# Optimization experiments

Hardware: AMD Instinct MI355X
Metric: run time of the kernel (lower is better)

Reference implementation:

```python
import jax, jax.numpy as jnp
import numpy as np

N = 100000
E = 6400000
GAMMA = 1.0
SUPPORT = 0.05


def cohesion_kernel(q, h):
    # piecewise Akinci cohesion kernel (Cd normalization is unused in the original)
    qm1_3_q3 = (q - 1.0) ** 3 * q ** 3
    k1 = 128.0 * qm1_3_q3 + 1.0   # q <= 0.5
    k2 = 64.0 * qm1_3_q3           # q > 0.5
    return -jnp.where(q <= 0.5, k1, k2)


def kernel_gradient(q, dist, h):
    # 2D Wendland C2 kernel gradient: W = 7/(pi h^2) (1-q)^4 (1+4q)
    C = 7.0 / (np.pi * h ** 2)
    dWdq = C * (-20.0 * q * jnp.clip(1.0 - q, 0.0, None) ** 3) / h
    return dWdq[:, None] * dist  # [E,2]


def setup_inputs() -> dict:
    key = jax.random.key(0)
    k1, k2, k3, k4, k5, k6, k7 = jax.random.split(key, 7)
    neighbors = jnp.stack([
        jax.random.randint(k1, (E,), 0, N),
        jax.random.randint(k2, (E,), 0, N),
    ], axis=0)  # [2,E] int
    fluidAreas = jax.random.uniform(k3, (N,), dtype=jnp.float32)
    fluidDensities = jax.random.uniform(k4, (N,), dtype=jnp.float32) + 0.5  # avoid div-by-0
    fluidRestDensity = jax.random.uniform(k5, (N,), dtype=jnp.float32) + 0.5
    fluidRadialDistances = jax.random.uniform(k6, (E,), dtype=jnp.float32)  # q in [0,1]
    fluidDistances = jax.random.normal(k7, (E, 2), dtype=jnp.float32)
    # normalize to unit direction vectors as in the SPH pipeline
    fluidDistances = fluidDistances / (jnp.linalg.norm(fluidDistances, axis=1, keepdims=True) + 1e-7)
    return {
        'neighbors': neighbors,
        'fluidAreas': fluidAreas,
        'fluidDensities': fluidDensities,
        'fluidRestDensity': fluidRestDensity,
        'fluidRadialDistances': fluidRadialDistances,
        'fluidDistances': fluidDistances,
    }


def reference(neighbors, fluidAreas, fluidDensities, fluidRestDensity,
              fluidRadialDistances, fluidDistances):
    i = neighbors[0]
    j = neighbors[1]

    # computeNormalFunction
    fac_n = fluidAreas[j] / fluidDensities[j]                  # [E]
    grad = kernel_gradient(fluidRadialDistances, fluidDistances, SUPPORT)  # [E,2]
    normals = SUPPORT * jax.ops.segment_sum(fac_n[:, None] * grad, i, num_segments=N)  # [N,2]

    # computeCurvatureForce
    curvature = -GAMMA * jax.ops.segment_sum(normals[i] - normals[j], i, num_segments=N)

    # computeCohesionForce
    fac_c = fluidAreas[j] * fluidRestDensity[j]                # [E]
    kern = cohesion_kernel(fluidRadialDistances, SUPPORT)      # [E]
    cohesion = -GAMMA * jax.ops.segment_sum((fac_c * kern)[:, None] * fluidDistances, i, num_segments=N)

    # both forces are accumulated into fluidAcceleration
    return curvature + cohesion
```

## Files before the change

### kernel.cpp

```cpp
#include <hip/hip_runtime.h>

constexpr int N_PART = 100000;
constexpr int N_EDGE = 6400000;
constexpr float SUPPORT = 0.05f;
constexpr float PI_F = 3.14159265358979323846f;

constexpr int CH_LOG2 = 12;
constexpr int CH      = 1 << CH_LOG2;
constexpr int NCH     = (N_EDGE + CH - 1) / CH;
constexpr int BIN_LOG2 = 13;
constexpr int BINSZ   = 1 << BIN_LOG2;
constexpr int NBIN    = (N_PART + BINSZ - 1) / BINSZ;
constexpr int G_MAX   = 39;
constexpr int ST_NW   = 8;

__global__ __launch_bounds__(512) void prep_fac(
    const float* __restrict__ areas,
    const float* __restrict__ dens,
    const float* __restrict__ rest,
    float2* __restrict__ fac)
{
    int p = blockIdx.x * blockDim.x + threadIdx.x;
    if (p < N_PART)
        fac[p] = make_float2(areas[p] / dens[p], areas[p] * rest[p]);
}

__global__ __launch_bounds__(512) void l1_sort(
    const int* __restrict__ nb,
    const float2* __restrict__ fac,
    const float* __restrict__ q,
    const float2* __restrict__ dist,
    unsigned* __restrict__ gpack,
    float2* __restrict__ gpay1,
    float2* __restrict__ gpay2,
    unsigned* __restrict__ btab)
{
    __shared__ unsigned rec_pack[CH];
    __shared__ float    rec_q[CH];
    __shared__ float    rec_dx[CH];
    __shared__ float    rec_dy[CH];
    __shared__ unsigned hist[ST_NW * NBIN];
    __shared__ unsigned curw[ST_NW * NBIN];
    __shared__ unsigned base[NBIN + 1];
    __shared__ unsigned bcnt[NBIN];

    const int t   = blockIdx.x;
    const int c0  = t * CH;
    const int len = min(CH, N_EDGE - c0);
    const int tid = threadIdx.x;
    const int wid = tid >> 6;

    for (int k = tid; k < ST_NW * NBIN; k += 512) hist[k] = 0u;

    unsigned iv[8], jv[8];
    float    qv[8], dxv[8], dyv[8];
    #pragma unroll
    for (int k = 0; k < 8; ++k) {
        int idx = tid + k * 512;
        if (idx < len) {
            iv[k] = (unsigned)nb[c0 + idx];
            jv[k] = (unsigned)nb[N_EDGE + c0 + idx];
            qv[k] = q[c0 + idx];
            float2 d = dist[c0 + idx];
            dxv[k] = d.x;
            dyv[k] = d.y;
        }
    }
    __syncthreads();

    #pragma unroll
    for (int k = 0; k < 8; ++k) {
        int idx = tid + k * 512;
        if (idx < len)
            atomicAdd(&hist[wid * NBIN + (iv[k] >> BIN_LOG2)], 1u);
    }
    __syncthreads();

    if (tid < NBIN) {
        unsigned run = 0;
        for (int w = 0; w < ST_NW; ++w) {
            curw[w * NBIN + tid] = run;
            run += hist[w * NBIN + tid];
        }
        bcnt[tid] = run;
    }
    __syncthreads();
    if (tid == 0) {
        unsigned run = 0;
        for (int b = 0; b < NBIN; ++b) { base[b] = run; run += bcnt[b]; }
        base[NBIN] = run;
    }
    __syncthreads();
    if (tid < ST_NW * NBIN) curw[tid] += base[tid % NBIN];
    if (tid < NBIN)  btab[t * 16 + tid]  = base[tid];
    if (tid == NBIN) btab[t * 16 + NBIN] = (unsigned)len;
    __syncthreads();

    #pragma unroll
    for (int k = 0; k < 8; ++k) {
        int idx = tid + k * 512;
        if (idx < len) {
            unsigned i   = iv[k];
            unsigned bin = i >> BIN_LOG2;
            unsigned r = atomicAdd(&curw[wid * NBIN + bin], 1u) & (CH - 1);
            rec_pack[r] = ((i & (BINSZ - 1)) << 17) | jv[k];
            rec_q[r]    = qv[k];
            rec_dx[r]   = dxv[k];
            rec_dy[r]   = dyv[k];
        }
    }
    __syncthreads();

    const float Cw = 7.0f / (PI_F * SUPPORT * SUPPORT);
    for (int p = tid; p < len; p += 512) {
        unsigned pack = rec_pack[p];
        float qq = rec_q[p];
        float dx = rec_dx[p], dy = rec_dy[p];
        unsigned j = pack & 0x1FFFFu;
        float2 f = fac[j];

        float omq  = fmaxf(1.0f - qq, 0.0f);
        float dWdq = Cw * (-20.0f * qq * omq * omq * omq) * (1.0f / SUPPORT);
        float s    = SUPPORT * f.x * dWdq;

        float qm1  = qq - 1.0f;
        float tt   = qm1 * qm1 * qm1 * qq * qq * qq;
        float kern = (qq <= 0.5f) ? fmaf(128.0f, tt, 1.0f) : 64.0f * tt;
        float fc   = f.y * kern;

        int o = c0 + p;
        gpack[o] = pack;
        gpay1[o] = make_float2(s * dx, s * dy);
        gpay2[o] = make_float2(fc * dx, fc * dy);
    }
}

__global__ __launch_bounds__(512) void passB(
    const unsigned* __restrict__ btab,
    const unsigned* __restrict__ gpack,
    const float2* __restrict__ gpay1,
    float2* __restrict__ partials,
    int G)
{
    __shared__ float accx[BINSZ];
    __shared__ float accy[BINSZ];
    const int b = blockIdx.x % NBIN;
    const int g = blockIdx.x / NBIN;
    const int wave = threadIdx.x >> 6;
    const int lane = threadIdx.x & 63;

    for (int k = threadIdx.x; k < BINSZ; k += 512) { accx[k] = 0.0f; accy[k] = 0.0f; }
    __syncthreads();

    const int t0 = (int)((long long)g * NCH / G);
    const int t1 = (int)((long long)(g + 1) * NCH / G);
    for (int t = t0 + wave; t < t1; t += 8) {
        const int c0  = t * CH;
        const unsigned ln = min(btab[t * 16 + NBIN], (unsigned)CH);
        unsigned sb = min(btab[t * 16 + b], ln);
        unsigned se = min(btab[t * 16 + b + 1], ln);
        for (unsigned k = sb + lane; k < se; k += 64) {
            int o = c0 + (int)k;
            unsigned pk = gpack[o];
            float2 p = gpay1[o];
            unsigned loc = (pk >> 17) & (BINSZ - 1);
            atomicAdd(&accx[loc], p.x);
            atomicAdd(&accy[loc], p.y);
        }
    }
    __syncthreads();

    float2* __restrict__ dst = partials + (size_t)g * (NBIN * BINSZ) + (size_t)b * BINSZ;
    for (int k = threadIdx.x; k < BINSZ; k += 512)
        dst[k] = make_float2(accx[k], accy[k]);
}

__global__ __launch_bounds__(512) void passD(
    const unsigned* __restrict__ btab,
    const unsigned* __restrict__ gpack,
    const float2* __restrict__ gpay2,
    const float2* __restrict__ normals,
    float2* __restrict__ partials,
    int G)
{
    __shared__ float accx[BINSZ];
    __shared__ float accy[BINSZ];
    const int b = blockIdx.x % NBIN;
    const int g = blockIdx.x / NBIN;
    const int wave = threadIdx.x >> 6;
    const int lane = threadIdx.x & 63;

    for (int k = threadIdx.x; k < BINSZ; k += 512) { accx[k] = 0.0f; accy[k] = 0.0f; }
    __syncthreads();

    const int gbase = b * BINSZ;
    const int t0 = (int)((long long)g * NCH / G);
    const int t1 = (int)((long long)(g + 1) * NCH / G);
    for (int t = t0 + wave; t < t1; t += 8) {
        const int c0  = t * CH;
        const unsigned ln = min(btab[t * 16 + NBIN], (unsigned)CH);
        unsigned sb = min(btab[t * 16 + b], ln);
        unsigned se = min(btab[t * 16 + b + 1], ln);
        for (unsigned k = sb + lane; k < se; k += 64) {
            int o = c0 + (int)k;
            unsigned pk = gpack[o];
            float2 coh = gpay2[o];
            unsigned loc = (pk >> 17) & (BINSZ - 1);
            unsigned j   = min(pk & 0x1FFFFu, (unsigned)(N_PART - 1));
            unsigned ii  = min((unsigned)(gbase + loc), (unsigned)(N_PART - 1));
            float2 nj = normals[j];
            float2 ni = normals[ii];
            atomicAdd(&accx[loc], nj.x - ni.x + coh.x);
            atomicAdd(&accy[loc], nj.y - ni.y + coh.y);
        }
    }
    __syncthreads();

    float2* __restrict__ dst = partials + (size_t)g * (NBIN * BINSZ) + (size_t)b * BINSZ;
    for (int k = threadIdx.x; k < BINSZ; k += 512)
        dst[k] = make_float2(accx[k], accy[k]);
}

__global__ __launch_bounds__(256) void reduceG(
    const float2* __restrict__ partials, float2* __restrict__ dst, int G)
{
    int p = blockIdx.x * blockDim.x + threadIdx.x;
    if (p >= N_PART) return;
    float ax = 0.0f, ay = 0.0f;
    for (int g = 0; g < G; ++g) {
        float2 v = partials[(size_t)g * (NBIN * BINSZ) + p];
        ax += v.x; ay += v.y;
    }
    dst[p] = make_float2(ax, ay);
}

constexpr int FB_BSZ_LOG2 = 13;
constexpr int FB_BSZ   = 1 << FB_BSZ_LOG2;
constexpr int FB_NBINS = (N_PART + FB_BSZ - 1) / FB_BSZ;
constexpr int FB_NP_PAD = FB_NBINS * FB_BSZ;
constexpr int FB_C_TARGET = 39;

__global__ __launch_bounds__(1024) void fb_pass1_binned(
    const int* __restrict__ nb, const float* __restrict__ areas,
    const float* __restrict__ dens, const float* __restrict__ q,
    const float2* __restrict__ dist, float* __restrict__ partials, int C)
{
    __shared__ float lds[2 * FB_BSZ];
    const int b = blockIdx.x % FB_NBINS;
    const int c = blockIdx.x / FB_NBINS;
    for (int k = threadIdx.x; k < 2 * FB_BSZ; k += blockDim.x) lds[k] = 0.0f;
    __syncthreads();
    const int start = (int)((long long)c       * (N_EDGE / 4) / C) * 4;
    const int end   = (int)((long long)(c + 1) * (N_EDGE / 4) / C) * 4;
    const int4* __restrict__ nb4 = (const int4*)nb;
    const float Cw = 7.0f / (PI_F * SUPPORT * SUPPORT);
    for (int e = start + (int)threadIdx.x * 4; e < end; e += (int)blockDim.x * 4) {
        int4 iq = nb4[e >> 2];
        #pragma unroll
        for (int k = 0; k < 4; ++k) {
            int iv = (k == 0) ? iq.x : (k == 1) ? iq.y : (k == 2) ? iq.z : iq.w;
            if ((iv >> FB_BSZ_LOG2) == b) {
                int ee = e + k;
                int j  = nb[N_EDGE + ee];
                float qq  = q[ee];
                float fac = areas[j] / dens[j];
                float omq  = fmaxf(1.0f - qq, 0.0f);
                float dWdq = Cw * (-20.0f * qq * omq * omq * omq) * (1.0f / SUPPORT);
                float s = SUPPORT * fac * dWdq;
                float2 d = dist[ee];
                int loc = (iv & (FB_BSZ - 1)) << 1;
                atomicAdd(&lds[loc],     s * d.x);
                atomicAdd(&lds[loc + 1], s * d.y);
            }
        }
    }
    __syncthreads();
    float2* __restrict__ dst = (float2*)partials + (size_t)c * FB_NP_PAD + (size_t)b * FB_BSZ;
    const float2* __restrict__ src = (const float2*)lds;
    for (int k = threadIdx.x; k < FB_BSZ; k += blockDim.x) dst[k] = src[k];
}

__global__ __launch_bounds__(1024) void fb_pass2_binned(
    const int* __restrict__ nb, const float* __restrict__ areas,
    const float* __restrict__ rest, const float* __restrict__ q,
    const float2* __restrict__ dist, const float2* __restrict__ normals,
    float* __restrict__ partials, int C)
{
    __shared__ float lds[2 * FB_BSZ];
    const int b = blockIdx.x % FB_NBINS;
    const int c = blockIdx.x / FB_NBINS;
    for (int k = threadIdx.x; k < 2 * FB_BSZ; k += blockDim.x) lds[k] = 0.0f;
    __syncthreads();
    const int start = (int)((long long)c       * (N_EDGE / 4) / C) * 4;
    const int end   = (int)((long long)(c + 1) * (N_EDGE / 4) / C) * 4;
    const int4* __restrict__ nb4 = (const int4*)nb;
    for (int e = start + (int)threadIdx.x * 4; e < end; e += (int)blockDim.x * 4) {
        int4 iq = nb4[e >> 2];
        #pragma unroll
        for (int k = 0; k < 4; ++k) {
            int iv = (k == 0) ? iq.x : (k == 1) ? iq.y : (k == 2) ? iq.z : iq.w;
            if ((iv >> FB_BSZ_LOG2) == b) {
                int ee = e + k;
                int j  = nb[N_EDGE + ee];
                float2 ni = normals[iv];
                float2 nj = normals[j];
                float qq  = q[ee];
                float fc  = areas[j] * rest[j];
                float qm1 = qq - 1.0f;
                float t   = qm1 * qm1 * qm1 * qq * qq * qq;
                float kern = (qq <= 0.5f) ? fmaf(128.0f, t, 1.0f) : 64.0f * t;
                float2 d = dist[ee];
                int loc = (iv & (FB_BSZ - 1)) << 1;
                atomicAdd(&lds[loc],     -(ni.x - nj.x) + fc * kern * d.x);
                atomicAdd(&lds[loc + 1], -(ni.y - nj.y) + fc * kern * d.y);
            }
        }
    }
    __syncthreads();
    float2* __restrict__ dst = (float2*)partials + (size_t)c * FB_NP_PAD + (size_t)b * FB_BSZ;
    const float2* __restrict__ src = (const float2*)lds;
    for (int k = threadIdx.x; k < FB_BSZ; k += blockDim.x) dst[k] = src[k];
}

__global__ __launch_bounds__(256) void fb_reduce_partials(
    const float* __restrict__ partials, float* __restrict__ dst, int C)
{
    int p = blockIdx.x * blockDim.x + threadIdx.x;
    if (p >= N_PART) return;
    const float2* __restrict__ p2 = (const float2*)partials;
    float ax = 0.0f, ay = 0.0f;
    for (int c = 0; c < C; ++c) {
        float2 v = p2[(size_t)c * FB_NP_PAD + p];
        ax += v.x; ay += v.y;
    }
    ((float2*)dst)[p] = make_float2(ax, ay);
}

__global__ __launch_bounds__(256) void fb_zero2(float* __restrict__ a,
                                                float* __restrict__ b, int n) {
    int idx = blockIdx.x * blockDim.x + threadIdx.x;
    if (idx < n) { a[idx] = 0.0f; b[idx] = 0.0f; }
}

__global__ __launch_bounds__(256) void fb_pass1_atomic(
    const int* __restrict__ nb, const float* __restrict__ areas,
    const float* __restrict__ dens, const float* __restrict__ q,
    const float2* __restrict__ dist, float* __restrict__ normals)
{
    int e = blockIdx.x * blockDim.x + threadIdx.x;
    if (e >= N_EDGE) return;
    int i = nb[e];
    int j = nb[N_EDGE + e];
    float qq  = q[e];
    float fac = areas[j] / dens[j];
    const float Cw = 7.0f / (PI_F * SUPPORT * SUPPORT);
    float omq  = fmaxf(1.0f - qq, 0.0f);
    float dWdq = Cw * (-20.0f * qq * omq * omq * omq) * (1.0f / SUPPORT);
    float s = SUPPORT * fac * dWdq;
    float2 d = dist[e];
    atomicAdd(&normals[2 * i],     s * d.x);
    atomicAdd(&normals[2 * i + 1], s * d.y);
}

__global__ __launch_bounds__(256) void fb_pass2_atomic(
    const int* __restrict__ nb, const float* __restrict__ areas,
    const float* __restrict__ rest, const float* __restrict__ q,
    const float2* __restrict__ dist, const float2* __restrict__ normals,
    float* __restrict__ out)
{
    int e = blockIdx.x * blockDim.x + threadIdx.x;
    if (e >= N_EDGE) return;
    int i = nb[e];
    int j = nb[N_EDGE + e];
    float2 ni = normals[i];
    float2 nj = normals[j];
    float qq  = q[e];
    float fc  = areas[j] * rest[j];
    float qm1 = qq - 1.0f;
    float t   = qm1 * qm1 * qm1 * qq * qq * qq;
    float kern = (qq <= 0.5f) ? fmaf(128.0f, t, 1.0f) : 64.0f * t;
    float2 d = dist[e];
    atomicAdd(&out[2 * i],     -(ni.x - nj.x) + fc * kern * d.x);
    atomicAdd(&out[2 * i + 1], -(ni.y - nj.y) + fc * kern * d.y);
}

extern "C" void kernel_launch(void* const* d_in, const int* in_sizes, int n_in,
                              void* d_out, int out_size, void* d_ws, size_t ws_size,
                              hipStream_t stream) {
    const int*   nb    = (const int*)d_in[0];
    const float* areas = (const float*)d_in[1];
    const float* dens  = (const float*)d_in[2];
    const float* rest  = (const float*)d_in[3];
    const float* q     = (const float*)d_in[4];
    const float* dist  = (const float*)d_in[5];
    float* out = (float*)d_out;

    size_t off = 0;
    auto take = [&](size_t bytes) { size_t o = off; off += (bytes + 255) & ~(size_t)255; return o; };
    size_t o_pack    = take((size_t)N_EDGE * sizeof(unsigned));
    size_t o_pay1    = take((size_t)N_EDGE * sizeof(float2));
    size_t o_pay2    = take((size_t)N_EDGE * sizeof(float2));
    size_t o_btab    = take((size_t)NCH * 16 * sizeof(unsigned));
    size_t o_normals = take((size_t)N_PART * sizeof(float2));
    size_t o_fac     = take((size_t)N_PART * sizeof(float2));
    size_t base_need = off;
    const size_t per_g = (size_t)(NBIN * BINSZ) * sizeof(float2);

    int G = 0;
    if (ws_size > base_need) {
        G = (int)((ws_size - base_need) / per_g);
        if (G > G_MAX) G = G_MAX;
    }

    char* ws = (char*)d_ws;

    if (G >= 6) {
        unsigned* gpack   = (unsigned*)(ws + o_pack);
        float2*   gpay1   = (float2*)(ws + o_pay1);
        float2*   gpay2   = (float2*)(ws + o_pay2);
        unsigned* btab    = (unsigned*)(ws + o_btab);
        float2*   normals = (float2*)(ws + o_normals);
        float2*   fac     = (float2*)(ws + o_fac);
        float2*   partials= (float2*)(ws + base_need);

        prep_fac<<<(N_PART + 511) / 512, 512, 0, stream>>>(areas, dens, rest, fac);
        l1_sort<<<NCH, 512, 0, stream>>>(
            nb, fac, q, (const float2*)dist,
            gpack, gpay1, gpay2, btab);
        passB<<<NBIN * G, 512, 0, stream>>>(btab, gpack, gpay1, partials, G);
        reduceG<<<(N_PART + 255) / 256, 256, 0, stream>>>(partials, normals, G);
        passD<<<NBIN * G, 512, 0, stream>>>(btab, gpack, gpay2, normals, partials, G);
        reduceG<<<(N_PART + 255) / 256, 256, 0, stream>>>(partials, (float2*)out, G);
        return;
    }

    const size_t normals_pad = 1 << 20;
    float* normals  = (float*)d_ws;
    float* partials = (float*)((char*)d_ws + normals_pad);
    const size_t per_chunk = (size_t)FB_NP_PAD * 2 * sizeof(float);
    int C = 0;
    if (ws_size > normals_pad) {
        C = (int)((ws_size - normals_pad) / per_chunk);
        if (C > FB_C_TARGET) C = FB_C_TARGET;
    }

    if (C >= 4) {
        const int grid = FB_NBINS * C;
        fb_pass1_binned<<<grid, 1024, 0, stream>>>(
            nb, areas, dens, q, (const float2*)dist, partials, C);
        fb_reduce_partials<<<(N_PART + 255) / 256, 256, 0, stream>>>(partials, normals, C);
        fb_pass2_binned<<<grid, 1024, 0, stream>>>(
            nb, areas, rest, q, (const float2*)dist, (const float2*)normals, partials, C);
        fb_reduce_partials<<<(N_PART + 255) / 256, 256, 0, stream>>>(partials, out, C);
    } else {
        const int nv = 2 * N_PART;
        fb_zero2<<<(nv + 255) / 256, 256, 0, stream>>>(normals, out, nv);
        const int blocks = (N_EDGE + 255) / 256;
        fb_pass1_atomic<<<blocks, 256, 0, stream>>>(
            nb, areas, dens, q, (const float2*)dist, normals);
        fb_pass2_atomic<<<blocks, 256, 0, stream>>>(
            nb, areas, rest, q, (const float2*)dist, (const float2*)normals, out);
    }
}
```

Baseline: 373.9 us.

## Replace partial buffers and reduce kernels with global atomic flush; halve bin size

The binned accumulation passes now flush their LDS accumulators straight into the global normals and output arrays with atomicAdd, instead of writing per-group partial buffers and running separate reduceG kernels. The bin size drops from 8192 to 4096, doubling the bin count and halving LDS per block. Each block also stages its per-chunk bin offsets in LDS. This removes two kernel launches and the partial-buffer traffic, at the cost of a zeroing kernel, global atomic contention across the fixed 40 groups, and non-deterministic summation order.

```diff
diff --git a/kernel.cpp b/kernel.cpp
--- a/kernel.cpp
+++ b/kernel.cpp
@@ -8,11 +8,13 @@
 constexpr int CH_LOG2 = 12;
 constexpr int CH      = 1 << CH_LOG2;
 constexpr int NCH     = (N_EDGE + CH - 1) / CH;
-constexpr int BIN_LOG2 = 13;
+constexpr int BIN_LOG2 = 12;
 constexpr int BINSZ   = 1 << BIN_LOG2;
 constexpr int NBIN    = (N_PART + BINSZ - 1) / BINSZ;
-constexpr int G_MAX   = 39;
+constexpr int BT_STRIDE = 32;
+constexpr int G_ACC   = 40;
 constexpr int ST_NW   = 8;
+constexpr int MAXC    = 48;
 
 __global__ __launch_bounds__(512) void prep_fac(
     const float* __restrict__ areas,
@@ -23,6 +25,12 @@
     int p = blockIdx.x * blockDim.x + threadIdx.x;
     if (p < N_PART)
         fac[p] = make_float2(areas[p] / dens[p], areas[p] * rest[p]);
+}
+
+__global__ __launch_bounds__(256) void zero2(float* __restrict__ a,
+                                             float* __restrict__ b, int n) {
+    int idx = blockIdx.x * blockDim.x + threadIdx.x;
+    if (idx < n) { a[idx] = 0.0f; b[idx] = 0.0f; }
 }
 
 __global__ __launch_bounds__(512) void l1_sort(
@@ -92,8 +100,8 @@
     }
     __syncthreads();
     if (tid < ST_NW * NBIN) curw[tid] += base[tid % NBIN];
-    if (tid < NBIN)  btab[t * 16 + tid]  = base[tid];
-    if (tid == NBIN) btab[t * 16 + NBIN] = (unsigned)len;
+    if (tid < NBIN)  btab[t * BT_STRIDE + tid]  = base[tid];
+    if (tid == NBIN) btab[t * BT_STRIDE + NBIN] = (unsigned)len;
     __syncthreads();
 
     #pragma unroll
@@ -139,26 +147,33 @@
     const unsigned* __restrict__ btab,
     const unsigned* __restrict__ gpack,
     const float2* __restrict__ gpay1,
-    float2* __restrict__ partials,
-    int G)
+    float* __restrict__ gnorm)
 {
     __shared__ float accx[BINSZ];
     __shared__ float accy[BINSZ];
+    __shared__ unsigned s_sb[MAXC], s_se[MAXC], s_ln[MAXC];
     const int b = blockIdx.x % NBIN;
     const int g = blockIdx.x / NBIN;
     const int wave = threadIdx.x >> 6;
     const int lane = threadIdx.x & 63;
 
+    const int t0 = (int)((long long)g * NCH / G_ACC);
+    const int t1 = (int)((long long)(g + 1) * NCH / G_ACC);
+    const int nt = t1 - t0;
+
     for (int k = threadIdx.x; k < BINSZ; k += 512) { accx[k] = 0.0f; accy[k] = 0.0f; }
-    __syncthreads();
-
-    const int t0 = (int)((long long)g * NCH / G);
-    const int t1 = (int)((long long)(g + 1) * NCH / G);
-    for (int t = t0 + wave; t < t1; t += 8) {
-        const int c0  = t * CH;
-        const unsigned ln = min(btab[t * 16 + NBIN], (unsigned)CH);
-        unsigned sb = min(btab[t * 16 + b], ln);
-        unsigned se = min(btab[t * 16 + b + 1], ln);
+    for (int c = threadIdx.x; c < nt; c += 512) {
+        s_sb[c] = btab[(t0 + c) * BT_STRIDE + b];
+        s_se[c] = btab[(t0 + c) * BT_STRIDE + b + 1];
+        s_ln[c] = btab[(t0 + c) * BT_STRIDE + NBIN];
+    }
+    __syncthreads();
+
+    for (int c = wave; c < nt; c += 8) {
+        const int c0  = (t0 + c) * CH;
+        const unsigned ln = min(s_ln[c], (unsigned)CH);
+        unsigned sb = min(s_sb[c], ln);
+        unsigned se = min(s_se[c], ln);
         for (unsigned k = sb + lane; k < se; k += 64) {
             int o = c0 + (int)k;
             unsigned pk = gpack[o];
@@ -170,9 +185,14 @@
     }
     __syncthreads();
 
-    float2* __restrict__ dst = partials + (size_t)g * (NBIN * BINSZ) + (size_t)b * BINSZ;
-    for (int k = threadIdx.x; k < BINSZ; k += 512)
-        dst[k] = make_float2(accx[k], accy[k]);
+    const int gbase = b * BINSZ;
+    for (int k = threadIdx.x; k < BINSZ; k += 512) {
+        int p = gbase + k;
+        if (p < N_PART) {
+            atomicAdd(&gnorm[2 * p],     accx[k]);
+            atomicAdd(&gnorm[2 * p + 1], accy[k]);
+        }
+    }
 }
 
 __global__ __launch_bounds__(512) void passD(
@@ -180,27 +200,34 @@
     const unsigned* __restrict__ gpack,
     const float2* __restrict__ gpay2,
     const float2* __restrict__ normals,
-    float2* __restrict__ partials,
-    int G)
+    float* __restrict__ gout)
 {
     __shared__ float accx[BINSZ];
     __shared__ float accy[BINSZ];
+    __shared__ unsigned s_sb[MAXC], s_se[MAXC], s_ln[MAXC];
     const int b = blockIdx.x % NBIN;
     const int g = blockIdx.x / NBIN;
     const int wave = threadIdx.x >> 6;
     const int lane = threadIdx.x & 63;
 
+    const int t0 = (int)((long long)g * NCH / G_ACC);
+    const int t1 = (int)((long long)(g + 1) * NCH / G_ACC);
+    const int nt = t1 - t0;
+
     for (int k = threadIdx.x; k < BINSZ; k += 512) { accx[k] = 0.0f; accy[k] = 0.0f; }
+    for (int c = threadIdx.x; c < nt; c += 512) {
+        s_sb[c] = btab[(t0 + c) * BT_STRIDE + b];
+        s_se[c] = btab[(t0 + c) * BT_STRIDE + b + 1];
+        s_ln[c] = btab[(t0 + c) * BT_STRIDE + NBIN];
+    }
     __syncthreads();
 
     const int gbase = b * BINSZ;
-    const int t0 = (int)((long long)g * NCH / G);
-    const int t1 = (int)((long long)(g + 1) * NCH / G);
-    for (int t = t0 + wave; t < t1; t += 8) {
-        const int c0  = t * CH;
-        const unsigned ln = min(btab[t * 16 + NBIN], (unsigned)CH);
-        unsigned sb = min(btab[t * 16 + b], ln);
-        unsigned se = min(btab[t * 16 + b + 1], ln);
+    for (int c = wave; c < nt; c += 8) {
+        const int c0  = (t0 + c) * CH;
+        const unsigned ln = min(s_ln[c], (unsigned)CH);
+        unsigned sb = min(s_sb[c], ln);
+        unsigned se = min(s_se[c], ln);
         for (unsigned k = sb + lane; k < se; k += 64) {
             int o = c0 + (int)k;
             unsigned pk = gpack[o];
@@ -216,22 +243,13 @@
     }
     __syncthreads();
 
-    float2* __restrict__ dst = partials + (size_t)g * (NBIN * BINSZ) + (size_t)b * BINSZ;
-    for (int k = threadIdx.x; k < BINSZ; k += 512)
-        dst[k] = make_float2(accx[k], accy[k]);
-}
-
-__global__ __launch_bounds__(256) void reduceG(
-    const float2* __restrict__ partials, float2* __restrict__ dst, int G)
-{
-    int p = blockIdx.x * blockDim.x + threadIdx.x;
-    if (p >= N_PART) return;
-    float ax = 0.0f, ay = 0.0f;
-    for (int g = 0; g < G; ++g) {
-        float2 v = partials[(size_t)g * (NBIN * BINSZ) + p];
-        ax += v.x; ay += v.y;
-    }
-    dst[p] = make_float2(ax, ay);
+    for (int k = threadIdx.x; k < BINSZ; k += 512) {
+        int p = gbase + k;
+        if (p < N_PART) {
+            atomicAdd(&gout[2 * p],     accx[k]);
+            atomicAdd(&gout[2 * p + 1], accy[k]);
+        }
+    }
 }
 
 constexpr int FB_BSZ_LOG2 = 13;
@@ -336,12 +354,6 @@
     ((float2*)dst)[p] = make_float2(ax, ay);
 }
 
-__global__ __launch_bounds__(256) void fb_zero2(float* __restrict__ a,
-                                                float* __restrict__ b, int n) {
-    int idx = blockIdx.x * blockDim.x + threadIdx.x;
-    if (idx < n) { a[idx] = 0.0f; b[idx] = 0.0f; }
-}
-
 __global__ __launch_bounds__(256) void fb_pass1_atomic(
     const int* __restrict__ nb, const float* __restrict__ areas,
     const float* __restrict__ dens, const float* __restrict__ q,
@@ -400,37 +412,29 @@
     size_t o_pack    = take((size_t)N_EDGE * sizeof(unsigned));
     size_t o_pay1    = take((size_t)N_EDGE * sizeof(float2));
     size_t o_pay2    = take((size_t)N_EDGE * sizeof(float2));
-    size_t o_btab    = take((size_t)NCH * 16 * sizeof(unsigned));
+    size_t o_btab    = take((size_t)NCH * BT_STRIDE * sizeof(unsigned));
     size_t o_normals = take((size_t)N_PART * sizeof(float2));
     size_t o_fac     = take((size_t)N_PART * sizeof(float2));
     size_t base_need = off;
-    const size_t per_g = (size_t)(NBIN * BINSZ) * sizeof(float2);
-
-    int G = 0;
-    if (ws_size > base_need) {
-        G = (int)((ws_size - base_need) / per_g);
-        if (G > G_MAX) G = G_MAX;
-    }
 
     char* ws = (char*)d_ws;
 
-    if (G >= 6) {
+    if (ws_size >= base_need) {
         unsigned* gpack   = (unsigned*)(ws + o_pack);
         float2*   gpay1   = (float2*)(ws + o_pay1);
         float2*   gpay2   = (float2*)(ws + o_pay2);
         unsigned* btab    = (unsigned*)(ws + o_btab);
         float2*   normals = (float2*)(ws + o_normals);
         float2*   fac     = (float2*)(ws + o_fac);
-        float2*   partials= (float2*)(ws + base_need);
-
+
+        zero2<<<(2 * N_PART + 255) / 256, 256, 0, stream>>>(
+            (float*)normals, out, 2 * N_PART);
         prep_fac<<<(N_PART + 511) / 512, 512, 0, stream>>>(areas, dens, rest, fac);
         l1_sort<<<NCH, 512, 0, stream>>>(
             nb, fac, q, (const float2*)dist,
             gpack, gpay1, gpay2, btab);
-        passB<<<NBIN * G, 512, 0, stream>>>(btab, gpack, gpay1, partials, G);
-        reduceG<<<(N_PART + 255) / 256, 256, 0, stream>>>(partials, normals, G);
-        passD<<<NBIN * G, 512, 0, stream>>>(btab, gpack, gpay2, normals, partials, G);
-        reduceG<<<(N_PART + 255) / 256, 256, 0, stream>>>(partials, (float2*)out, G);
+        passB<<<NBIN * G_ACC, 512, 0, stream>>>(btab, gpack, gpay1, (float*)normals);
+        passD<<<NBIN * G_ACC, 512, 0, stream>>>(btab, gpack, gpay2, normals, out);
         return;
     }
 
@@ -454,7 +458,7 @@
         fb_reduce_partials<<<(N_PART + 255) / 256, 256, 0, stream>>>(partials, out, C);
     } else {
         const int nv = 2 * N_PART;
-        fb_zero2<<<(nv + 255) / 256, 256, 0, stream>>>(normals, out, nv);
+        zero2<<<(nv + 255) / 256, 256, 0, stream>>>(normals, out, nv);
         const int blocks = (N_EDGE + 255) / 256;
         fb_pass1_atomic<<<blocks, 256, 0, stream>>>(
             nb, areas, dens, q, (const float2*)dist, normals);
```

Measured after the change: 389.0 us. +4.0%, slower.

## Halve bin size, use wave-ballot ranking, stage chunk offsets, unroll scatter loops

Applied to the files above, without the earlier changes.

Bins shrink from 8192 to 4096 particles, so there are 25 bins and each accumulation block holds smaller LDS arrays, which may allow more blocks per CU. The btab stride grows to 32 to fit the extra bins. In the sort kernel, the shared-memory atomic histogram and the atomic position counter are replaced by deterministic ballot/mbcnt ranking per wave, with per-k prefix tables held in LDS. The passB and passD kernels now preload each chunk's bin start and end offsets into LDS and unroll the edge loop by two to issue more loads at once. The costs are a longer per-element bin loop in the sort kernel, twice as many blocks in passB and passD, and less headroom in the G/MAXC sizing.

```diff
diff --git a/kernel.cpp b/kernel.cpp
--- a/kernel.cpp
+++ b/kernel.cpp
@@ -8,11 +8,13 @@
 constexpr int CH_LOG2 = 12;
 constexpr int CH      = 1 << CH_LOG2;
 constexpr int NCH     = (N_EDGE + CH - 1) / CH;
-constexpr int BIN_LOG2 = 13;
+constexpr int BIN_LOG2 = 12;
 constexpr int BINSZ   = 1 << BIN_LOG2;
 constexpr int NBIN    = (N_PART + BINSZ - 1) / BINSZ;
-constexpr int G_MAX   = 39;
+constexpr int BT_STRIDE = 32;
+constexpr int G_MAX   = 40;
 constexpr int ST_NW   = 8;
+constexpr int MAXC    = 272;
 
 __global__ __launch_bounds__(512) void prep_fac(
     const float* __restrict__ areas,
@@ -40,7 +42,8 @@
     __shared__ float    rec_dx[CH];
     __shared__ float    rec_dy[CH];
     __shared__ unsigned hist[ST_NW * NBIN];
-    __shared__ unsigned curw[ST_NW * NBIN];
+    __shared__ unsigned wbase[ST_NW * NBIN];
+    __shared__ unsigned kpre[ST_NW * 8 * NBIN];
     __shared__ unsigned base[NBIN + 1];
     __shared__ unsigned bcnt[NBIN];
 
@@ -49,8 +52,7 @@
     const int len = min(CH, N_EDGE - c0);
     const int tid = threadIdx.x;
     const int wid = tid >> 6;
-
-    for (int k = tid; k < ST_NW * NBIN; k += 512) hist[k] = 0u;
+    const int lane = tid & 63;
 
     unsigned iv[8], jv[8];
     float    qv[8], dxv[8], dyv[8];
@@ -66,20 +68,31 @@
             dyv[k] = d.y;
         }
     }
-    __syncthreads();
-
+
+    unsigned rnk[8];
+    unsigned cntb = 0;
     #pragma unroll
     for (int k = 0; k < 8; ++k) {
         int idx = tid + k * 512;
-        if (idx < len)
-            atomicAdd(&hist[wid * NBIN + (iv[k] >> BIN_LOG2)], 1u);
-    }
+        unsigned bin = (idx < len) ? (iv[k] >> BIN_LOG2) : 0xFFu;
+        if (lane < NBIN) kpre[(wid * 8 + k) * NBIN + lane] = cntb;
+        unsigned r = 0;
+        for (unsigned b = 0; b < (unsigned)NBIN; ++b) {
+            unsigned long long m = __ballot(bin == b);
+            unsigned lt = __builtin_amdgcn_mbcnt_hi((unsigned)(m >> 32),
+                          __builtin_amdgcn_mbcnt_lo((unsigned)m, 0u));
+            if (bin == b) r = lt;
+            if ((unsigned)lane == b) cntb += (unsigned)__popcll(m);
+        }
+        rnk[k] = r;
+    }
+    if (lane < NBIN) hist[wid * NBIN + lane] = cntb;
     __syncthreads();
 
     if (tid < NBIN) {
         unsigned run = 0;
         for (int w = 0; w < ST_NW; ++w) {
-            curw[w * NBIN + tid] = run;
+            wbase[w * NBIN + tid] = run;
             run += hist[w * NBIN + tid];
         }
         bcnt[tid] = run;
@@ -91,9 +104,9 @@
         base[NBIN] = run;
     }
     __syncthreads();
-    if (tid < ST_NW * NBIN) curw[tid] += base[tid % NBIN];
-    if (tid < NBIN)  btab[t * 16 + tid]  = base[tid];
-    if (tid == NBIN) btab[t * 16 + NBIN] = (unsigned)len;
+    if (tid < ST_NW * NBIN) wbase[tid] += base[tid % NBIN];
+    if (tid < NBIN)  btab[t * BT_STRIDE + tid]  = base[tid];
+    if (tid == NBIN) btab[t * BT_STRIDE + NBIN] = (unsigned)len;
     __syncthreads();
 
     #pragma unroll
@@ -102,11 +115,13 @@
         if (idx < len) {
             unsigned i   = iv[k];
             unsigned bin = i >> BIN_LOG2;
-            unsigned r = atomicAdd(&curw[wid * NBIN + bin], 1u) & (CH - 1);
-            rec_pack[r] = ((i & (BINSZ - 1)) << 17) | jv[k];
-            rec_q[r]    = qv[k];
-            rec_dx[r]   = dxv[k];
-            rec_dy[r]   = dyv[k];
+            unsigned pos = (wbase[wid * NBIN + bin]
+                          + kpre[(wid * 8 + k) * NBIN + bin]
+                          + rnk[k]) & (CH - 1);
+            rec_pack[pos] = ((i & (BINSZ - 1)) << 17) | jv[k];
+            rec_q[pos]    = qv[k];
+            rec_dx[pos]   = dxv[k];
+            rec_dy[pos]   = dyv[k];
         }
     }
     __syncthreads();
@@ -144,22 +159,39 @@
 {
     __shared__ float accx[BINSZ];
     __shared__ float accy[BINSZ];
+    __shared__ unsigned s_sb[MAXC], s_se[MAXC];
     const int b = blockIdx.x % NBIN;
     const int g = blockIdx.x / NBIN;
     const int wave = threadIdx.x >> 6;
     const int lane = threadIdx.x & 63;
 
-    for (int k = threadIdx.x; k < BINSZ; k += 512) { accx[k] = 0.0f; accy[k] = 0.0f; }
-    __syncthreads();
-
     const int t0 = (int)((long long)g * NCH / G);
     const int t1 = (int)((long long)(g + 1) * NCH / G);
-    for (int t = t0 + wave; t < t1; t += 8) {
-        const int c0  = t * CH;
-        const unsigned ln = min(btab[t * 16 + NBIN], (unsigned)CH);
-        unsigned sb = min(btab[t * 16 + b], ln);
-        unsigned se = min(btab[t * 16 + b + 1], ln);
-        for (unsigned k = sb + lane; k < se; k += 64) {
+    const int nt = t1 - t0;
+
+    for (int k = threadIdx.x; k < BINSZ; k += 512) { accx[k] = 0.0f; accy[k] = 0.0f; }
+    for (int c = threadIdx.x; c < nt; c += 512) {
+        s_sb[c] = btab[(t0 + c) * BT_STRIDE + b];
+        s_se[c] = btab[(t0 + c) * BT_STRIDE + b + 1];
+    }
+    __syncthreads();
+
+    for (int c = wave; c < nt; c += 8) {
+        const int c0  = (t0 + c) * CH;
+        unsigned sb = s_sb[c], se = s_se[c];
+        unsigned k = sb + lane;
+        for (; k + 64 < se; k += 128) {
+            int o0 = c0 + (int)k, o1 = o0 + 64;
+            unsigned pk0 = gpack[o0], pk1 = gpack[o1];
+            float2 p0 = gpay1[o0], p1 = gpay1[o1];
+            unsigned l0 = (pk0 >> 17) & (BINSZ - 1);
+            unsigned l1 = (pk1 >> 17) & (BINSZ - 1);
+            atomicAdd(&accx[l0], p0.x);
+            atomicAdd(&accy[l0], p0.y);
+            atomicAdd(&accx[l1], p1.x);
+            atomicAdd(&accy[l1], p1.y);
+        }
+        if (k < se) {
             int o = c0 + (int)k;
             unsigned pk = gpack[o];
             float2 p = gpay1[o];
@@ -185,28 +217,53 @@
 {
     __shared__ float accx[BINSZ];
     __shared__ float accy[BINSZ];
+    __shared__ unsigned s_sb[MAXC], s_se[MAXC];
     const int b = blockIdx.x % NBIN;
     const int g = blockIdx.x / NBIN;
     const int wave = threadIdx.x >> 6;
     const int lane = threadIdx.x & 63;
 
-    for (int k = threadIdx.x; k < BINSZ; k += 512) { accx[k] = 0.0f; accy[k] = 0.0f; }
-    __syncthreads();
-
-    const int gbase = b * BINSZ;
     const int t0 = (int)((long long)g * NCH / G);
     const int t1 = (int)((long long)(g + 1) * NCH / G);
-    for (int t = t0 + wave; t < t1; t += 8) {
-        const int c0  = t * CH;
-        const unsigned ln = min(btab[t * 16 + NBIN], (unsigned)CH);
-        unsigned sb = min(btab[t * 16 + b], ln);
-        unsigned se = min(btab[t * 16 + b + 1], ln);
-        for (unsigned k = sb + lane; k < se; k += 64) {
+    const int nt = t1 - t0;
+
+    for (int k = threadIdx.x; k < BINSZ; k += 512) { accx[k] = 0.0f; accy[k] = 0.0f; }
+    for (int c = threadIdx.x; c < nt; c += 512) {
+        s_sb[c] = btab[(t0 + c) * BT_STRIDE + b];
+        s_se[c] = btab[(t0 + c) * BT_STRIDE + b + 1];
+    }
+    __syncthreads();
+
+    const int gbase = b * BINSZ;
+    for (int c = wave; c < nt; c += 8) {
+        const int c0  = (t0 + c) * CH;
+        unsigned sb = s_sb[c], se = s_se[c];
+        unsigned k = sb + lane;
+        for (; k + 64 < se; k += 128) {
+            int o0 = c0 + (int)k, o1 = o0 + 64;
+            unsigned pk0 = gpack[o0], pk1 = gpack[o1];
+            float2 h0 = gpay2[o0], h1 = gpay2[o1];
+            unsigned j0 = min(pk0 & 0x1FFFFu, (unsigned)(N_PART - 1));
+            unsigned j1 = min(pk1 & 0x1FFFFu, (unsigned)(N_PART - 1));
+            unsigned l0 = (pk0 >> 17) & (BINSZ - 1);
+            unsigned l1 = (pk1 >> 17) & (BINSZ - 1);
+            unsigned i0 = min((unsigned)(gbase + l0), (unsigned)(N_PART - 1));
+            unsigned i1 = min((unsigned)(gbase + l1), (unsigned)(N_PART - 1));
+            float2 nj0 = normals[j0];
+            float2 nj1 = normals[j1];
+            float2 ni0 = normals[i0];
+            float2 ni1 = normals[i1];
+            atomicAdd(&accx[l0], nj0.x - ni0.x + h0.x);
+            atomicAdd(&accy[l0], nj0.y - ni0.y + h0.y);
+            atomicAdd(&accx[l1], nj1.x - ni1.x + h1.x);
+            atomicAdd(&accy[l1], nj1.y - ni1.y + h1.y);
+        }
+        if (k < se) {
             int o = c0 + (int)k;
             unsigned pk = gpack[o];
             float2 coh = gpay2[o];
+            unsigned j   = min(pk & 0x1FFFFu, (unsigned)(N_PART - 1));
             unsigned loc = (pk >> 17) & (BINSZ - 1);
-            unsigned j   = min(pk & 0x1FFFFu, (unsigned)(N_PART - 1));
             unsigned ii  = min((unsigned)(gbase + loc), (unsigned)(N_PART - 1));
             float2 nj = normals[j];
             float2 ni = normals[ii];
@@ -400,7 +457,7 @@
     size_t o_pack    = take((size_t)N_EDGE * sizeof(unsigned));
     size_t o_pay1    = take((size_t)N_EDGE * sizeof(float2));
     size_t o_pay2    = take((size_t)N_EDGE * sizeof(float2));
-    size_t o_btab    = take((size_t)NCH * 16 * sizeof(unsigned));
+    size_t o_btab    = take((size_t)NCH * BT_STRIDE * sizeof(unsigned));
     size_t o_normals = take((size_t)N_PART * sizeof(float2));
     size_t o_fac     = take((size_t)N_PART * sizeof(float2));
     size_t base_need = off;
```

Measured after the change: 384.7 us. 1.03x slower.
